# Optimization experiments

Hardware: AMD Instinct MI355X
Metric: run time of the kernel (lower is better)

The kernel has to match this reference:

```python
import jax, jax.numpy as jnp
import numpy as np

NUM_HEADS = 4

def setup_inputs() -> dict:
    key = jax.random.key(0)
    ks = jax.random.split(key, 8)
    B, C, H, W = 4, 256, 128, 128
    Cq = C // 8  # query/key channels
    x  = jax.random.normal(ks[0], (B, C, H, W), dtype=jnp.float32)
    Wq = jax.random.normal(ks[1], (Cq, C), dtype=jnp.float32) * 0.05
    bq = jax.random.normal(ks[2], (Cq,),  dtype=jnp.float32) * 0.01
    Wk = jax.random.normal(ks[3], (Cq, C), dtype=jnp.float32) * 0.05
    bk = jax.random.normal(ks[4], (Cq,),  dtype=jnp.float32) * 0.01
    Wv = jax.random.normal(ks[5], (C, C),  dtype=jnp.float32) * 0.05
    bv = jax.random.normal(ks[6], (C,),   dtype=jnp.float32) * 0.01
    # torch init is zeros; use a nonzero value so the attention path contributes
    gamma = jnp.array([0.5], dtype=jnp.float32)
    return {"x": x, "Wq": Wq, "bq": bq, "Wk": Wk, "bk": bk, "Wv": Wv, "bv": bv, "gamma": gamma}

def _conv1x1(x, Wm, b):
    # 1x1 conv == per-pixel linear map over channels
    return jnp.einsum('bchw,oc->bohw', x, Wm) + b[None, :, None, None]

def reference(x, Wq, bq, Wk, bk, Wv, bv, gamma):
    B, C, H, W = x.shape
    nh = NUM_HEADS
    # project, then fold heads into batch: (B*nh, c_head, H, W)
    q = _conv1x1(x, Wq, bq).reshape(B * nh, -1, H, W)
    k = _conv1x1(x, Wk, bk).reshape(B * nh, -1, H, W)
    v = _conv1x1(x, Wv, bv).reshape(B * nh, -1, H, W)
    # horizontal (row-wise) attention over W: energy [BH, H, W, W]
    e_h = jnp.einsum('bchw,bchv->bhwv', q, k)
    a_h = jax.nn.softmax(e_h, axis=-1)
    o_h = jnp.einsum('bhwv,bchv->bchw', a_h, v)  # (BH, cv, H, W)
    # vertical (column-wise) attention over H: energy [BH, W, H, H]
    e_v = jnp.einsum('bchw,bcgw->bwhg', q, k)
    a_v = jax.nn.softmax(e_v, axis=-1)
    # original permutes back as (BH, cv, W, H); requires H == W to add
    o_v = jnp.einsum('bwhg,bcgw->bcwh', a_v, v)
    attn = (o_h + o_v).reshape(B, C, H, W)
    return gamma * attn + x
```

## Files before the change

### kernel.cpp

```cpp
#include <hip/hip_runtime.h>

#define HW 16384

typedef __attribute__((ext_vector_type(8))) short short8;
typedef __attribute__((ext_vector_type(16))) float floatx16;
typedef __attribute__((ext_vector_type(4))) unsigned int uvec4;

__device__ inline unsigned short f2bf(float f) {
    unsigned u = __builtin_bit_cast(unsigned, f);
    u = (u + 0x7FFFu + ((u >> 16) & 1u)) >> 16;
    return (unsigned short)u;
}

__device__ inline unsigned pack_bf_trunc(float lo, float hi) {
    return __builtin_amdgcn_perm(__builtin_bit_cast(unsigned, hi),
                                 __builtin_bit_cast(unsigned, lo), 0x07060302u);
}

__global__ __launch_bounds__(256) void cast_xt_kernel(
    const float* __restrict__ x,
    const float* __restrict__ Wq, const float* __restrict__ Wk,
    const float* __restrict__ Wv, unsigned short* __restrict__ Wb,
    unsigned short* __restrict__ xt)
{
    __shared__ unsigned short T[64][66];
    const int tid = threadIdx.x;
    const int p0 = blockIdx.x * 64;
    const int c0 = blockIdx.y * 64;
    const int b  = blockIdx.z;

    if (b == 0 && blockIdx.y == 0 && blockIdx.x < 80) {
        int e0 = (blockIdx.x * 256 + tid) * 4;
        int row = e0 >> 8, col = e0 & 255;
        const float* src = (row < 32) ? (Wq + row * 256 + col)
                         : (row < 64) ? (Wk + (row - 32) * 256 + col)
                                      : (Wv + (row - 64) * 256 + col);
        float4 v = *(const float4*)src;
        if (row < 32) {
            const float L2E = 1.4426950408889634f;
            v.x *= L2E; v.y *= L2E; v.z *= L2E; v.w *= L2E;
        }
        uint2 pk;
        pk.x = f2bf(v.x) | ((unsigned)f2bf(v.y) << 16);
        pk.y = f2bf(v.z) | ((unsigned)f2bf(v.w) << 16);
        *(uint2*)&Wb[e0] = pk;
    }

    #pragma unroll
    for (int i = 0; i < 4; i++) {
        int e = i * 256 + tid;
        int c = e >> 4, seg = e & 15;
        float4 v = *(const float4*)&x[((b * 256 + c0 + c) << 14) + p0 + seg * 4];
        ((unsigned*)&T[c][seg * 4])[0] = f2bf(v.x) | ((unsigned)f2bf(v.y) << 16);
        ((unsigned*)&T[c][seg * 4])[1] = f2bf(v.z) | ((unsigned)f2bf(v.w) << 16);
    }
    __syncthreads();
    #pragma unroll
    for (int i = 0; i < 2; i++) {
        int e = i * 256 + tid;
        int p = e >> 3, cs = e & 7;
        unsigned short t[8];
        #pragma unroll
        for (int j = 0; j < 8; j++) t[j] = T[cs * 8 + j][p];
        uint4 pk;
        pk.x = t[0] | ((unsigned)t[1] << 16);
        pk.y = t[2] | ((unsigned)t[3] << 16);
        pk.z = t[4] | ((unsigned)t[5] << 16);
        pk.w = t[6] | ((unsigned)t[7] << 16);
        *(uint4*)&xt[(((b << 14) + p0 + p) << 8) + c0 + cs * 8] = pk;
    }
}

__global__ __launch_bounds__(256, 3) void proj_mfma_kernel(
    const unsigned short* __restrict__ Wb, const unsigned short* __restrict__ xt,
    const float* __restrict__ bq, const float* __restrict__ bk,
    const float* __restrict__ bv,
    unsigned short* __restrict__ qb, unsigned short* __restrict__ kb,
    unsigned short* __restrict__ vb)
{
    __shared__ __align__(16) unsigned short As[64 * 64];
    __shared__ __align__(16) unsigned short Bs[256 * 64];
    __shared__ float biasS[64];
    const int tid = threadIdx.x;
    const int p0  = blockIdx.x * 256;
    const int oc0 = blockIdx.y * 64;
    const int b   = blockIdx.z;
    const int w = tid >> 6, lr = tid & 31, lh = (tid & 63) >> 5;

    if (tid < 64) biasS[tid] = (oc0 == 0)
        ? ((tid < 32) ? bq[tid] * 1.4426950408889634f : bk[tid - 32])
        : bv[oc0 - 64 + tid];

    floatx16 z16 = {0,0,0,0,0,0,0,0,0,0,0,0,0,0,0,0};
    floatx16 acc[2][2] = {{z16, z16}, {z16, z16}};
    const int bpx = (b << 14) + p0;

    for (int kc = 0; kc < 256; kc += 64) {
        if (kc) __syncthreads();
        #pragma unroll
        for (int i = 0; i < 2; i++) {
            int e = i * 256 + tid;
            int row = e >> 3, seg = e & 7, cp = seg ^ (row & 7);
            *(uint4*)&As[row * 64 + cp * 8] =
                *(const uint4*)&Wb[(oc0 + row) * 256 + kc + seg * 8];
        }
        #pragma unroll
        for (int i = 0; i < 8; i++) {
            int e = i * 256 + tid;
            int row = e >> 3, seg = e & 7, cp = seg ^ (row & 7);
            *(uint4*)&Bs[row * 64 + cp * 8] =
                *(const uint4*)&xt[((bpx + row) << 8) + kc + seg * 8];
        }
        __syncthreads();
        #pragma unroll
        for (int ks = 0; ks < 4; ks++) {
            int c = 2 * ks + lh;
            int cx = (c ^ (lr & 7)) * 8;
            short8 af0 = *(const short8*)&As[lr * 64 + cx];
            short8 af1 = *(const short8*)&As[(32 + lr) * 64 + cx];
            short8 bf0 = *(const short8*)&Bs[(64 * w + lr) * 64 + cx];
            short8 bf1 = *(const short8*)&Bs[(64 * w + 32 + lr) * 64 + cx];
            acc[0][0] = __builtin_amdgcn_mfma_f32_32x32x16_bf16(af0, bf0, acc[0][0], 0, 0, 0);
            acc[0][1] = __builtin_amdgcn_mfma_f32_32x32x16_bf16(af0, bf1, acc[0][1], 0, 0, 0);
            acc[1][0] = __builtin_amdgcn_mfma_f32_32x32x16_bf16(af1, bf0, acc[1][0], 0, 0, 0);
            acc[1][1] = __builtin_amdgcn_mfma_f32_32x32x16_bf16(af1, bf1, acc[1][1], 0, 0, 0);
        }
    }

    __syncthreads();
    if (oc0 == 0) {
        unsigned short* Cq = Bs;
        #pragma unroll
        for (int i = 0; i < 2; i++) {
            #pragma unroll
            for (int j = 0; j < 2; j++) {
                int px = 64 * w + 32 * j + lr;
                #pragma unroll
                for (int g = 0; g < 4; g++) {
                    float v0 = acc[i][j][4*g+0] + biasS[32*i + 8*g + 4*lh + 0];
                    float v1 = acc[i][j][4*g+1] + biasS[32*i + 8*g + 4*lh + 1];
                    float v2 = acc[i][j][4*g+2] + biasS[32*i + 8*g + 4*lh + 2];
                    float v3 = acc[i][j][4*g+3] + biasS[32*i + 8*g + 4*lh + 3];
                    uint2 u; u.x = pack_bf_trunc(v0, v1); u.y = pack_bf_trunc(v2, v3);
                    int cp = (4 * i + g) ^ (px & 7);
                    *(uint2*)&Cq[px * 64 + cp * 8 + 4 * lh] = u;
                }
            }
        }
        __syncthreads();
        #pragma unroll
        for (int i = 0; i < 8; i++) {
            int px = tid;
            int cp = i ^ (px & 7);
            uint4 val = *(const uint4*)&Cq[px * 64 + cp * 8];
            if (i < 4) *(uint4*)&qb[(unsigned)((b * 4 + i)     * HW + p0 + px) * 8] = val;
            else       *(uint4*)&kb[(unsigned)((b * 4 + i - 4) * HW + p0 + px) * 8] = val;
        }
    } else {
        unsigned short* Cv = Bs;
        #pragma unroll
        for (int i = 0; i < 2; i++) {
            #pragma unroll
            for (int j = 0; j < 2; j++) {
                int px = 64 * w + 32 * j + lr;
                #pragma unroll
                for (int reg = 0; reg < 16; reg++) {
                    int oc = 32 * i + (reg & 3) + 8 * (reg >> 2) + 4 * lh;
                    float v = acc[i][j][reg] + biasS[oc];
                    int cp = (px >> 3) ^ (oc & 31);
                    Cv[oc * 256 + cp * 8 + (px & 7)] =
                        (unsigned short)(__builtin_bit_cast(unsigned, v) >> 16);
                }
            }
        }
        __syncthreads();
        #pragma unroll
        for (int i = 0; i < 8; i++) {
            int u = i * 256 + tid;
            int oc = u >> 5, seg = u & 31;
            int cp = seg ^ (oc & 31);
            uint4 val = *(const uint4*)&Cv[oc * 256 + cp * 8];
            *(uint4*)&vb[(unsigned)(b * 256 + oc0 - 64 + oc) * HW + p0 + seg * 8] = val;
        }
    }
}

__global__ __launch_bounds__(256) void tqk_kernel(
    const unsigned short* __restrict__ qb, const unsigned short* __restrict__ kb,
    unsigned short* __restrict__ qt, unsigned short* __restrict__ kt)
{
    __shared__ uint4 t[32][33];
    const int plane = blockIdx.y;
    const int tile  = blockIdx.x;
    const int tx = tile & 3, ty = tile >> 2;
    const uint4* src = (const uint4*)(plane < 16 ? qb : kb) + (plane & 15) * HW;
    uint4*       dst = (uint4*)(plane < 16 ? qt : kt) + (plane & 15) * HW;
    const int c = threadIdx.x & 31, r0 = threadIdx.x >> 5;
    #pragma unroll
    for (int i = 0; i < 4; i++) {
        int r = r0 + i * 8;
        t[r][c] = src[(ty * 32 + r) * 128 + tx * 32 + c];
    }
    __syncthreads();
    #pragma unroll
    for (int i = 0; i < 4; i++) {
        int r = r0 + i * 8;
        dst[(tx * 32 + r) * 128 + ty * 32 + c] = t[c][r];
    }
}

__global__ __launch_bounds__(256) void tv_kernel(
    const unsigned short* __restrict__ vb, unsigned short* __restrict__ vt)
{
    __shared__ unsigned short T[64][66];
    const int plane = blockIdx.y;
    const int tile  = blockIdx.x;
    const int tx = tile & 1, ty = tile >> 1;
    const unsigned* src = (const unsigned*)(vb + plane * HW);
    unsigned*       dst = (unsigned*)(vt + plane * HW);
    const int tid = threadIdx.x;
    #pragma unroll
    for (int i = 0; i < 8; i++) {
        int e = i * 256 + tid;
        int r = e >> 5, cp = e & 31;
        *(unsigned*)&T[r][2 * cp] = src[(ty * 64 + r) * 64 + tx * 32 + cp];
    }
    __syncthreads();
    #pragma unroll
    for (int i = 0; i < 8; i++) {
        int e = i * 256 + tid;
        int c = e >> 5, rp = e & 31;
        unsigned lo = T[2 * rp][c], hi = T[2 * rp + 1][c];
        dst[(tx * 64 + c) * 64 + ty * 32 + rp] = lo | (hi << 16);
    }
}

__global__ __launch_bounds__(256, 2) void attn_kernel(
    const unsigned short* __restrict__ qb, const unsigned short* __restrict__ kb,
    const unsigned short* __restrict__ vb,
    const unsigned short* __restrict__ qt, const unsigned short* __restrict__ kt,
    const unsigned short* __restrict__ vt,
    const float* __restrict__ xin, const float* __restrict__ gamma,
    float* __restrict__ out)
{
    __shared__ __align__(16) unsigned short Vs[2][64 * 128];

    const int tid = threadIdx.x;
    const int y = blockIdx.x, bh = blockIdx.y;
    const int w = tid >> 6, l = tid & 63, lr = l & 31, lh = l >> 5;

    #pragma unroll
    for (int s = 0; s < 2; s++) {
        const unsigned short* vsrc = s ? vt : vb;
        #pragma unroll
        for (int i = 0; i < 4; i++) {
            int e = i * 256 + tid;
            int ch = e >> 4, sg = e & 15, sgp = sg ^ (ch & 15);
            *(uint4*)&Vs[s][ch * 128 + sgp * 8] =
                *(const uint4*)(vsrc + (bh * 64 + ch) * HW + y * 128 + sg * 8);
        }
    }
    __syncthreads();

    floatx16 z16 = {0,0,0,0,0,0,0,0,0,0,0,0,0,0,0,0};
    floatx16 oh0 = z16, oh1 = z16;
    floatx16 ov0 = z16, ov1 = z16;
    short8 z8 = {0,0,0,0,0,0,0,0};
    float ssA = 1.0f, ssB = 1.0f;

    #pragma unroll
    for (int stage = 0; stage < 2; stage++) {
        const unsigned short* qsrc = (stage ? qt : qb) + (bh * 128 + y) * 1024;
        const unsigned short* ksrc = (stage ? kt : kb) + (bh * 128 + y) * 1024;
        short8 bf = z8;
        if (lh == 0) bf = *(const short8*)(qsrc + (32 * w + lr) * 8);

        floatx16 et[4];
        #pragma unroll
        for (int kg = 0; kg < 4; kg++) {
            short8 af = z8;
            if (lh == 0) af = *(const short8*)(ksrc + (32 * kg + lr) * 8);
            et[kg] = __builtin_amdgcn_mfma_f32_32x32x16_bf16(af, bf, z16, 0, 0, 0);
        }

        float partial = 0.f;
        #pragma unroll
        for (int kg = 0; kg < 4; kg++) {
            floatx16 e = et[kg];
            #pragma unroll
            for (int r = 0; r < 16; r++) {
                float p = exp2f(e[r]);
                e[r] = p;
                partial += p;
            }
            #pragma unroll
            for (int cc = 0; cc < 2; cc++) {
                unsigned X0 = pack_bf_trunc(e[8*cc+0], e[8*cc+1]);
                unsigned X1 = pack_bf_trunc(e[8*cc+2], e[8*cc+3]);
                unsigned X2 = pack_bf_trunc(e[8*cc+4], e[8*cc+5]);
                unsigned X3 = pack_bf_trunc(e[8*cc+6], e[8*cc+7]);
                unsigned pX0 = __shfl_xor(X0, 32);
                unsigned pX1 = __shfl_xor(X1, 32);
                unsigned pX2 = __shfl_xor(X2, 32);
                unsigned pX3 = __shfl_xor(X3, 32);
                uvec4 t;
                t.x = lh ? pX2 : X0;
                t.y = lh ? pX3 : X1;
                t.z = lh ? X2  : pX0;
                t.w = lh ? X3  : pX1;
                short8 pf = __builtin_bit_cast(short8, t);
                int ks = 2 * kg + cc;
                int cp = ((2 * ks + lh) ^ (lr & 15)) * 8;
                short8 v0 = *(const short8*)&Vs[stage][lr * 128 + cp];
                short8 v1 = *(const short8*)&Vs[stage][(32 + lr) * 128 + cp];
                if (stage == 0) {
                    oh0 = __builtin_amdgcn_mfma_f32_32x32x16_bf16(v0, pf, oh0, 0, 0, 0);
                    oh1 = __builtin_amdgcn_mfma_f32_32x32x16_bf16(v1, pf, oh1, 0, 0, 0);
                } else {
                    ov0 = __builtin_amdgcn_mfma_f32_32x32x16_bf16(v0, pf, ov0, 0, 0, 0);
                    ov1 = __builtin_amdgcn_mfma_f32_32x32x16_bf16(v1, pf, ov1, 0, 0, 0);
                }
            }
        }
        float ssum = partial + __shfl_xor(partial, 32);
        if (stage == 0) ssA = ssum; else ssB = ssum;
    }

    __syncthreads();

    const float g  = gamma[0];
    const float g0 = g / ssA, g1 = g / ssB;
    const int xq = 32 * w + lr;
    #pragma unroll
    for (int reg = 0; reg < 16; reg++) {
        int ch = (reg & 3) + 8 * (reg >> 2) + 4 * lh;
        int idx0 = (bh * 64 + ch) * HW + y * 128 + xq;
        int idx1 = (bh * 64 + 32 + ch) * HW + y * 128 + xq;
        out[idx0] = g0 * oh0[reg] + g1 * ov0[reg] + xin[idx0];
        out[idx1] = g0 * oh1[reg] + g1 * ov1[reg] + xin[idx1];
    }
}

extern "C" void kernel_launch(void* const* d_in, const int* in_sizes, int n_in,
                              void* d_out, int out_size, void* d_ws, size_t ws_size,
                              hipStream_t stream) {
    const float* x     = (const float*)d_in[0];
    const float* Wq    = (const float*)d_in[1];
    const float* bq    = (const float*)d_in[2];
    const float* Wk    = (const float*)d_in[3];
    const float* bk    = (const float*)d_in[4];
    const float* Wv    = (const float*)d_in[5];
    const float* bv    = (const float*)d_in[6];
    const float* gamma = (const float*)d_in[7];
    float* out = (float*)d_out;

    unsigned short* Wb   = (unsigned short*)d_ws;
    unsigned short* qb16 = Wb + 320 * 256;
    unsigned short* kb16 = qb16 + 16 * HW * 8;
    unsigned short* qt16 = kb16 + 16 * HW * 8;
    unsigned short* kt16 = qt16 + 16 * HW * 8;
    unsigned short* vb16 = kt16 + 16 * HW * 8;
    unsigned short* vt16 = vb16 + 1024 * HW;
    unsigned short* xt = (unsigned short*)d_out;

    cast_xt_kernel<<<dim3(256, 4, 4), 256, 0, stream>>>(x, Wq, Wk, Wv, Wb, xt);
    proj_mfma_kernel<<<dim3(64, 5, 4), 256, 0, stream>>>(Wb, xt, bq, bk, bv, qb16, kb16, vb16);
    tqk_kernel<<<dim3(16, 32), 256, 0, stream>>>(qb16, kb16, qt16, kt16);
    tv_kernel<<<dim3(4, 1024), 256, 0, stream>>>(vb16, vt16);
    attn_kernel<<<dim3(128, 16), 256, 0, stream>>>(qb16, kb16, vb16, qt16, kt16, vt16, x, gamma, out);
}
```

Before: 198.9 us.

## Drop Q/K transpose kernel and remap blocks for XCD-aware scheduling

Removes the tqk transpose kernel. The attention kernel now reads Q and K directly in strided column order for the vertical stage, instead of from pre-transposed copies. Proj and attn launches are flattened to 1D grids, and block IDs are swizzled so consecutive logical tiles land on the same XCD (blockIdx&7 round-robin), aiming for better L2 locality. This saves a launch plus a round trip through global memory. The cost is strided 16-byte gathers (stride 128 pixels) in the vertical stage, which may be less coalesced.

Measured after the change: 199.8 us. About the same (+0.5%).

```diff
diff --git a/kernel.cpp b/kernel.cpp
--- a/kernel.cpp
+++ b/kernel.cpp
@@ -82,9 +82,12 @@
     __shared__ __align__(16) unsigned short Bs[256 * 64];
     __shared__ float biasS[64];
     const int tid = threadIdx.x;
-    const int p0  = blockIdx.x * 256;
-    const int oc0 = blockIdx.y * 64;
-    const int b   = blockIdx.z;
+    const int logical = (blockIdx.x & 7) * 160 + (blockIdx.x >> 3);
+    const int y5 = logical % 5;
+    const int pb = logical / 5;
+    const int p0  = (pb & 63) * 256;
+    const int oc0 = y5 * 64;
+    const int b   = pb >> 6;
     const int w = tid >> 6, lr = tid & 31, lh = (tid & 63) >> 5;
 
     if (tid < 64) biasS[tid] = (oc0 == 0)
@@ -185,30 +188,6 @@
     }
 }
 
-__global__ __launch_bounds__(256) void tqk_kernel(
-    const unsigned short* __restrict__ qb, const unsigned short* __restrict__ kb,
-    unsigned short* __restrict__ qt, unsigned short* __restrict__ kt)
-{
-    __shared__ uint4 t[32][33];
-    const int plane = blockIdx.y;
-    const int tile  = blockIdx.x;
-    const int tx = tile & 3, ty = tile >> 2;
-    const uint4* src = (const uint4*)(plane < 16 ? qb : kb) + (plane & 15) * HW;
-    uint4*       dst = (uint4*)(plane < 16 ? qt : kt) + (plane & 15) * HW;
-    const int c = threadIdx.x & 31, r0 = threadIdx.x >> 5;
-    #pragma unroll
-    for (int i = 0; i < 4; i++) {
-        int r = r0 + i * 8;
-        t[r][c] = src[(ty * 32 + r) * 128 + tx * 32 + c];
-    }
-    __syncthreads();
-    #pragma unroll
-    for (int i = 0; i < 4; i++) {
-        int r = r0 + i * 8;
-        dst[(tx * 32 + r) * 128 + ty * 32 + c] = t[c][r];
-    }
-}
-
 __global__ __launch_bounds__(256) void tv_kernel(
     const unsigned short* __restrict__ vb, unsigned short* __restrict__ vt)
 {
@@ -238,7 +217,6 @@
 __global__ __launch_bounds__(256, 2) void attn_kernel(
     const unsigned short* __restrict__ qb, const unsigned short* __restrict__ kb,
     const unsigned short* __restrict__ vb,
-    const unsigned short* __restrict__ qt, const unsigned short* __restrict__ kt,
     const unsigned short* __restrict__ vt,
     const float* __restrict__ xin, const float* __restrict__ gamma,
     float* __restrict__ out)
@@ -246,7 +224,8 @@
     __shared__ __align__(16) unsigned short Vs[2][64 * 128];
 
     const int tid = threadIdx.x;
-    const int y = blockIdx.x, bh = blockIdx.y;
+    const int logical = (blockIdx.x & 7) * 256 + (blockIdx.x >> 3);
+    const int y = logical & 127, bh = logical >> 7;
     const int w = tid >> 6, l = tid & 63, lr = l & 31, lh = l >> 5;
 
     #pragma unroll
@@ -268,18 +247,27 @@
     short8 z8 = {0,0,0,0,0,0,0,0};
     float ssA = 1.0f, ssB = 1.0f;
 
+    const unsigned short* qpl = qb + bh * (HW * 8);
+    const unsigned short* kpl = kb + bh * (HW * 8);
+
     #pragma unroll
     for (int stage = 0; stage < 2; stage++) {
-        const unsigned short* qsrc = (stage ? qt : qb) + (bh * 128 + y) * 1024;
-        const unsigned short* ksrc = (stage ? kt : kb) + (bh * 128 + y) * 1024;
         short8 bf = z8;
-        if (lh == 0) bf = *(const short8*)(qsrc + (32 * w + lr) * 8);
+        if (lh == 0) {
+            int px = 32 * w + lr;
+            int off = stage ? (px * 128 + y) : (y * 128 + px);
+            bf = *(const short8*)(qpl + off * 8);
+        }
 
         floatx16 et[4];
         #pragma unroll
         for (int kg = 0; kg < 4; kg++) {
             short8 af = z8;
-            if (lh == 0) af = *(const short8*)(ksrc + (32 * kg + lr) * 8);
+            if (lh == 0) {
+                int px = 32 * kg + lr;
+                int off = stage ? (px * 128 + y) : (y * 128 + px);
+                af = *(const short8*)(kpl + off * 8);
+            }
             et[kg] = __builtin_amdgcn_mfma_f32_32x32x16_bf16(af, bf, z16, 0, 0, 0);
         }
 
@@ -362,10 +350,10 @@
     unsigned short* vb16 = kt16 + 16 * HW * 8;
     unsigned short* vt16 = vb16 + 1024 * HW;
     unsigned short* xt = (unsigned short*)d_out;
+    (void)qt16; (void)kt16;
 
     cast_xt_kernel<<<dim3(256, 4, 4), 256, 0, stream>>>(x, Wq, Wk, Wv, Wb, xt);
-    proj_mfma_kernel<<<dim3(64, 5, 4), 256, 0, stream>>>(Wb, xt, bq, bk, bv, qb16, kb16, vb16);
-    tqk_kernel<<<dim3(16, 32), 256, 0, stream>>>(qb16, kb16, qt16, kt16);
+    proj_mfma_kernel<<<dim3(1280), 256, 0, stream>>>(Wb, xt, bq, bk, bv, qb16, kb16, vb16);
     tv_kernel<<<dim3(4, 1024), 256, 0, stream>>>(vb16, vt16);
-    attn_kernel<<<dim3(128, 16), 256, 0, stream>>>(qb16, kb16, vb16, qt16, kt16, vt16, x, gamma, out);
-}
+    attn_kernel<<<dim3(2048), 256, 0, stream>>>(qb16, kb16, vb16, vt16, x, gamma, out);
+}
```
